# Optimization experiments

Hardware: AMD Instinct MI355X
Metric: run time of the kernel (lower is better)

## Reference

```python
import jax, jax.numpy as jnp
import numpy as np
import math

HIDDEN = 768
NUM_HEADS = 12
HEAD_DIM = HIDDEN // NUM_HEADS
EPS = 1e-05
MU_LEARNED = 0.0    # registered buffer init value (inference mode)
SIGMA_LEARNED = 1.0 # registered buffer init value (inference mode)
SCALES = (0.5, 1.0, 2.0)


def make_pe(n, d):
    # Sinusoidal positional encoding, identical to PositionalEncoding buffer.
    pos = np.arange(n, dtype=np.float32)[:, None]
    div = np.exp(np.arange(0, d, 2, dtype=np.float32) * (-math.log(10000.0) / d))
    pe = np.zeros((n, d), dtype=np.float32)
    pe[:, 0::2] = np.sin(pos * div)
    pe[:, 1::2] = np.cos(pos * div)
    return jnp.asarray(pe)


def setup_inputs() -> dict:
    key = jax.random.key(0)
    ks = jax.random.split(key, 12)
    B, C, Hh, Ww = 8, 256, 32, 32
    feat = jax.random.normal(ks[0], (B, C, Hh, Ww), jnp.float32)
    I = jax.random.uniform(ks[1], (B, 1, Hh, Ww), jnp.float32)
    sc_c = 1.0 / math.sqrt(C)
    sd = 1.0 / math.sqrt(HIDDEN)
    proj_w = jax.random.normal(ks[2], (C, HIDDEN), jnp.float32) * sc_c  # 1x1 conv as matmul
    proj_b = jnp.zeros((HIDDEN,), jnp.float32)
    wq = jax.random.normal(ks[3], (HIDDEN, HIDDEN), jnp.float32) * sd
    bq = jnp.zeros((HIDDEN,), jnp.float32)
    wk = jax.random.normal(ks[4], (HIDDEN, HIDDEN), jnp.float32) * sd
    bk = jnp.zeros((HIDDEN,), jnp.float32)
    wv = jax.random.normal(ks[5], (HIDDEN, HIDDEN), jnp.float32) * sd
    bv = jnp.zeros((HIDDEN,), jnp.float32)
    wo = jax.random.normal(ks[6], (HIDDEN, HIDDEN), jnp.float32) * sd
    bo = jnp.zeros((HIDDEN,), jnp.float32)
    lam = jnp.float32(0.5)
    return dict(feat=feat, I=I, proj_w=proj_w, proj_b=proj_b,
                wq=wq, bq=bq, wk=wk, bk=bk, wv=wv, bv=bv, wo=wo, bo=bo, lam=lam)


def reference(feat, I, proj_w, proj_b, wq, bq, wk, bk, wv, bv, wo, bo, lam):
    B, C, Hh, Ww = feat.shape
    N = Hh * Ww
    # HiddenFeatureProjection: 1x1 conv projection -> flatten -> tokens [B, N, D]
    tokens = jnp.einsum('bchw,cd->bhwd', feat, proj_w).reshape(B, N, HIDDEN) + proj_b
    tokens = tokens + make_pe(N, HIDDEN)[None]
    # GaussianWeightModule (inference path, learned buffers mu=0, sigma=1)
    G = sum(jnp.exp(-(I - MU_LEARNED) ** 2 / (2.0 * (k * SIGMA_LEARNED) ** 2 + EPS))
            for k in SCALES) / float(len(SCALES))  # [B,1,H,W]
    g = G.reshape(B, N)                              # H*W == N by construction
    bias = g[:, :, None] * g[:, None, :]             # [B, N, N] outer product
    # GaussianEnhancedAttention
    q = (tokens @ wq + bq).reshape(B, N, NUM_HEADS, HEAD_DIM).transpose(0, 2, 1, 3)
    k = (tokens @ wk + bk).reshape(B, N, NUM_HEADS, HEAD_DIM).transpose(0, 2, 1, 3)
    v = (tokens @ wv + bv).reshape(B, N, NUM_HEADS, HEAD_DIM).transpose(0, 2, 1, 3)
    scores = jnp.einsum('bhnd,bhmd->bhnm', q, k) / math.sqrt(HEAD_DIM)
    scores = scores + lam * bias[:, None, :, :]
    attn = jax.nn.softmax(scores, axis=-1)
    out = jnp.einsum('bhnm,bhmd->bhnd', attn, v).transpose(0, 2, 1, 3).reshape(B, N, HIDDEN)
    return out @ wo + bo
```

## Files before the change

kernel.cpp:

```cpp
#include <hip/hip_runtime.h>
#include <hip/hip_bf16.h>
#include <math.h>

#define HIDDEN 768
#define NHEADS 12
#define HDIM   64
#define NTOK   1024
#define BATCH  8
#define CIN    256
#define M_ALL  (BATCH * NTOK)
#define LSTR   72

typedef __hip_bfloat16 bf16;
typedef short frag8 __attribute__((ext_vector_type(8)));
typedef short s16x4 __attribute__((ext_vector_type(4)));
typedef unsigned int u32x2 __attribute__((ext_vector_type(2)));
typedef float f32x4 __attribute__((ext_vector_type(4)));

#define GL2LDS(gp, lp) \
    __builtin_amdgcn_global_load_lds((const __attribute__((address_space(1))) void*)(gp), \
                                     (__attribute__((address_space(3))) void*)(lp), 16, 0, 0)

__device__ __forceinline__ short f2bs(float x){
    union { bf16 h; short s; } u; u.h = __float2bfloat16(x); return u.s;
}

__device__ __forceinline__ float gaussw(float x){
    float x2 = x * x;
    return (__expf(-x2 / 0.50001f) + __expf(-x2 / 2.00001f) + __expf(-x2 / 8.00001f)) * (1.0f / 3.0f);
}

__global__ __launch_bounds__(256) void prep_all(
    const float* __restrict__ proj_w, const float* __restrict__ feat,
    short* __restrict__ wtp, short* __restrict__ featT, float* __restrict__ pe)
{
    const int blk = blockIdx.x;
    const int tid = threadIdx.x;
    if (blk >= 560) {
        const float kfac = -9.210340371976184f / 768.0f;
        int e0 = (blk - 560) * 3072 + tid;
        #pragma unroll
        for (int it = 0; it < 12; it++) {
            int e = e0 + it * 256;
            int n = e / 768;
            int d = e - n * 768;
            float ang = (float)n * expf((float)(2 * (d >> 1)) * kfac);
            pe[e] = (d & 1) ? cosf(ang) : sinf(ang);
        }
        return;
    }
    __shared__ short t[64][65];
    const float* W; short* WT; int K, N, k0, n0;
    if (blk < 48) {
        W = proj_w; WT = wtp;
        K = CIN; N = HIDDEN; k0 = (blk / 12) * 64; n0 = (blk % 12) * 64;
    } else {
        int rem = blk - 48;
        int b = rem / 64; rem %= 64;
        W = feat + (size_t)b * CIN * NTOK; WT = featT + (size_t)b * NTOK * CIN;
        K = CIN; N = NTOK; k0 = (rem / 16) * 64; n0 = (rem % 16) * 64;
    }
    #pragma unroll
    for (int it = 0; it < 16; it++) {
        int e = tid + 256 * it;
        int kk = e / 64, nn = e % 64;
        t[kk][nn] = f2bs(W[(size_t)(k0 + kk) * N + n0 + nn]);
    }
    __syncthreads();
    #pragma unroll
    for (int it = 0; it < 16; it++) {
        int e = tid + 256 * it;
        int nn = e / 64, kk = e % 64;
        WT[(size_t)(n0 + nn) * K + k0 + kk] = t[kk][nn];
    }
}

__global__ __launch_bounds__(256) void tokens_wprep(
    const short* __restrict__ A, const short* __restrict__ WT,
    const float* __restrict__ bias, const float* __restrict__ pe,
    short* __restrict__ outv,
    const float* __restrict__ wq, const float* __restrict__ wk,
    const float* __restrict__ wv, const float* __restrict__ wo,
    short* __restrict__ wtqkv)
{
    const int blk = blockIdx.x;
    const int tid = threadIdx.x;
    if (blk >= 768) {
        __shared__ short t[64][65];
        int bw = blk - 768;
        int p = bw / 144, rem = bw % 144;
        const float* srcs[4] = {wq, wk, wv, wo};
        const float* W = srcs[p];
        short* WTo = wtqkv + (size_t)p * HIDDEN * HIDDEN;
        int k0 = (rem / 12) * 64, n0 = (rem % 12) * 64;
        #pragma unroll
        for (int it = 0; it < 16; it++) {
            int e = tid + 256 * it;
            int kk = e / 64, nn = e % 64;
            t[kk][nn] = f2bs(W[(size_t)(k0 + kk) * HIDDEN + n0 + nn]);
        }
        __syncthreads();
        #pragma unroll
        for (int it = 0; it < 16; it++) {
            int e = tid + 256 * it;
            int nn = e / 64, kk = e % 64;
            WTo[(size_t)(n0 + nn) * HIDDEN + k0 + kk] = t[kk][nn];
        }
        return;
    }
    __shared__ short Al[64 * 32];
    __shared__ short Bl[128 * 32];
    const int m0   = (blk & 127) * 64;
    const int n0   = (blk >> 7) * 128;
    const int lane = tid & 63, wid = tid >> 6;
    const int wn   = wid * 32;
    const int l16  = lane & 15, quad = lane >> 4;

    const int sr  = lane >> 2;
    const int ssg = (lane & 3) ^ ((sr >> 1) & 3);
    const int fsw = (l16 >> 1) & 3;

    const f32x4 z4 = {0.f, 0.f, 0.f, 0.f};
    f32x4 acc[4][2];
    #pragma unroll
    for (int i = 0; i < 4; i++)
        #pragma unroll
        for (int j = 0; j < 2; j++) acc[i][j] = z4;

    const int K = CIN;
    for (int k0 = 0; k0 < K; k0 += 32) {
        GL2LDS(A + (size_t)(m0 + wid * 16 + sr) * K + k0 + ssg * 8, &Al[(wid * 16) * 32]);
        #pragma unroll
        for (int t = 0; t < 2; t++) {
            int rbase = wid * 32 + t * 16;
            GL2LDS(WT + (size_t)(n0 + rbase + sr) * K + k0 + ssg * 8, &Bl[rbase * 32]);
        }
        __syncthreads();
        frag8 af[4], bfr[2];
        #pragma unroll
        for (int i = 0; i < 4; i++)
            af[i]  = *(const frag8*)&Al[(i * 16 + l16) * 32 + ((quad ^ fsw) * 8)];
        #pragma unroll
        for (int j = 0; j < 2; j++)
            bfr[j] = *(const frag8*)&Bl[(wn + j * 16 + l16) * 32 + ((quad ^ fsw) * 8)];
        #pragma unroll
        for (int i = 0; i < 4; i++)
            #pragma unroll
            for (int j = 0; j < 2; j++)
                acc[i][j] = __builtin_amdgcn_mfma_f32_16x16x32_bf16(af[i], bfr[j], acc[i][j], 0, 0, 0);
        __syncthreads();
    }

    #pragma unroll
    for (int i = 0; i < 4; i++) {
        #pragma unroll
        for (int r = 0; r < 4; r++) {
            int m = m0 + i * 16 + quad * 4 + r;
            int n_tok = m & (NTOK - 1);
            #pragma unroll
            for (int j = 0; j < 2; j++) {
                int col = n0 + wn + j * 16 + l16;
                float val = acc[i][j][r] + bias[col] + pe[n_tok * HIDDEN + col];
                outv[(size_t)m * HIDDEN + col] = f2bs(val);
            }
        }
    }
}

__global__ __launch_bounds__(256) void transpose_v(
    const short* __restrict__ v, short* __restrict__ vT,
    const float* __restrict__ I, float* __restrict__ g)
{
    if (blockIdx.y == BATCH * NHEADS) {
        int idx = blockIdx.x * 512 + threadIdx.x * 2;
        g[idx]     = gaussw(I[idx]);
        g[idx + 1] = gaussw(I[idx + 1]);
        return;
    }
    __shared__ short t[64][65];
    const int nt = blockIdx.x;
    const int bh = blockIdx.y;
    const int b = bh / NHEADS, h = bh % NHEADS;
    const int tid = threadIdx.x;
    #pragma unroll
    for (int it = 0; it < 16; it++) {
        int e = tid + 256 * it;
        int rr = e / 64, cc = e % 64;
        t[rr][cc] = v[(size_t)(b * NTOK + nt * 64 + rr) * HIDDEN + h * HDIM + cc];
    }
    __syncthreads();
    #pragma unroll
    for (int it = 0; it < 16; it++) {
        int e = tid + 256 * it;
        int c2 = e / 64, r2 = e % 64;
        vT[((size_t)bh * HDIM + c2) * NTOK + nt * 64 + r2] = t[r2][c2];
    }
}

__global__ __launch_bounds__(256) void gemm_mfma128(
    const short* __restrict__ A, const short* __restrict__ WT0, long wt_z,
    const float* __restrict__ b0, const float* __restrict__ b1, const float* __restrict__ b2,
    short* o0, short* o1, short* o2, int K)
{
    __shared__ short Al[2][128 * 32];
    __shared__ short Bl[2][128 * 32];
    const int z = blockIdx.z;
    const short* WT  = WT0 + (size_t)z * wt_z;
    const float* bias = (z == 0) ? b0 : (z == 1) ? b1 : b2;
    short* outv       = (z == 0) ? o0 : (z == 1) ? o1 : o2;

    const int tid  = threadIdx.x;
    const int m0   = blockIdx.x * 128;
    const int n0   = blockIdx.y * 128;
    const int lane = tid & 63, wid = tid >> 6;
    const int wm   = (wid >> 1) * 64, wn = (wid & 1) * 64;
    const int l16  = lane & 15, quad = lane >> 4;

    const int sr  = lane >> 2;
    const int ssg = (lane & 3) ^ ((sr >> 1) & 3);
    const int fsw = (l16 >> 1) & 3;

    const f32x4 z4 = {0.f, 0.f, 0.f, 0.f};
    f32x4 acc[4][4];
    #pragma unroll
    for (int i = 0; i < 4; i++)
        #pragma unroll
        for (int j = 0; j < 4; j++) acc[i][j] = z4;

    #pragma unroll
    for (int t = 0; t < 2; t++) {
        int rbase = wid * 32 + t * 16;
        int r = rbase + sr;
        GL2LDS(A  + (size_t)(m0 + r) * K + ssg * 8, &Al[0][rbase * 32]);
        GL2LDS(WT + (size_t)(n0 + r) * K + ssg * 8, &Bl[0][rbase * 32]);
    }
    __syncthreads();

    const int NSTEP = K / 32;
    for (int ks = 0; ks < NSTEP; ks++) {
        const int cur = ks & 1;
        if (ks < NSTEP - 1) {
            int k0n = (ks + 1) * 32;
            #pragma unroll
            for (int t = 0; t < 2; t++) {
                int rbase = wid * 32 + t * 16;
                int r = rbase + sr;
                GL2LDS(A  + (size_t)(m0 + r) * K + k0n + ssg * 8, &Al[cur ^ 1][rbase * 32]);
                GL2LDS(WT + (size_t)(n0 + r) * K + k0n + ssg * 8, &Bl[cur ^ 1][rbase * 32]);
            }
        }
        frag8 af[4], bfr[4];
        #pragma unroll
        for (int i = 0; i < 4; i++)
            af[i]  = *(const frag8*)&Al[cur][(wm + i * 16 + l16) * 32 + ((quad ^ fsw) * 8)];
        #pragma unroll
        for (int j = 0; j < 4; j++)
            bfr[j] = *(const frag8*)&Bl[cur][(wn + j * 16 + l16) * 32 + ((quad ^ fsw) * 8)];
        #pragma unroll
        for (int i = 0; i < 4; i++)
            #pragma unroll
            for (int j = 0; j < 4; j++)
                acc[i][j] = __builtin_amdgcn_mfma_f32_16x16x32_bf16(af[i], bfr[j], acc[i][j], 0, 0, 0);
        __syncthreads();
    }

    #pragma unroll
    for (int i = 0; i < 4; i++) {
        #pragma unroll
        for (int r = 0; r < 4; r++) {
            int m = m0 + wm + i * 16 + quad * 4 + r;
            #pragma unroll
            for (int j = 0; j < 4; j++) {
                int col = n0 + wn + j * 16 + l16;
                outv[(size_t)m * HIDDEN + col] = f2bs(acc[i][j][r] + bias[col]);
            }
        }
    }
}

__global__ __launch_bounds__(256) void gemm_mfma64f(
    const short* __restrict__ A, const short* __restrict__ WT,
    const float* __restrict__ bias, float* __restrict__ outv, int K)
{
    __shared__ short Al[64 * 32];
    __shared__ short Bl[128 * 32];
    const int tid  = threadIdx.x;
    const int m0   = blockIdx.x * 64;
    const int n0   = blockIdx.y * 128;
    const int lane = tid & 63, wid = tid >> 6;
    const int wn   = wid * 32;
    const int l16  = lane & 15, quad = lane >> 4;

    const int sr  = lane >> 2;
    const int ssg = (lane & 3) ^ ((sr >> 1) & 3);
    const int fsw = (l16 >> 1) & 3;

    const f32x4 z4 = {0.f, 0.f, 0.f, 0.f};
    f32x4 acc[4][2];
    #pragma unroll
    for (int i = 0; i < 4; i++)
        #pragma unroll
        for (int j = 0; j < 2; j++) acc[i][j] = z4;

    for (int k0 = 0; k0 < K; k0 += 32) {
        GL2LDS(A + (size_t)(m0 + wid * 16 + sr) * K + k0 + ssg * 8, &Al[(wid * 16) * 32]);
        #pragma unroll
        for (int t = 0; t < 2; t++) {
            int rbase = wid * 32 + t * 16;
            GL2LDS(WT + (size_t)(n0 + rbase + sr) * K + k0 + ssg * 8, &Bl[rbase * 32]);
        }
        __syncthreads();
        frag8 af[4], bfr[2];
        #pragma unroll
        for (int i = 0; i < 4; i++)
            af[i]  = *(const frag8*)&Al[(i * 16 + l16) * 32 + ((quad ^ fsw) * 8)];
        #pragma unroll
        for (int j = 0; j < 2; j++)
            bfr[j] = *(const frag8*)&Bl[(wn + j * 16 + l16) * 32 + ((quad ^ fsw) * 8)];
        #pragma unroll
        for (int i = 0; i < 4; i++)
            #pragma unroll
            for (int j = 0; j < 2; j++)
                acc[i][j] = __builtin_amdgcn_mfma_f32_16x16x32_bf16(af[i], bfr[j], acc[i][j], 0, 0, 0);
        __syncthreads();
    }

    #pragma unroll
    for (int i = 0; i < 4; i++) {
        #pragma unroll
        for (int r = 0; r < 4; r++) {
            int m = m0 + i * 16 + quad * 4 + r;
            #pragma unroll
            for (int j = 0; j < 2; j++) {
                int col = n0 + wn + j * 16 + l16;
                outv[(size_t)m * HIDDEN + col] = acc[i][j][r] + bias[col];
            }
        }
    }
}

__global__ __launch_bounds__(256, 3) void attn_mfma(
    const short* __restrict__ q, const short* __restrict__ k, const short* __restrict__ vT,
    const float* __restrict__ g, const float* __restrict__ lam_p, short* __restrict__ out)
{
    __shared__ short Pl[128 * LSTR];
    __shared__ short Ks[2][64 * 64];
    __shared__ short Vt[2][64 * 64];

    const int tid  = threadIdx.x;
    const int lin  = blockIdx.x;
    const int xcd  = lin & 7, slot = lin >> 3;
    const int b    = xcd;
    const int h    = slot >> 3;
    const int qt   = slot & 7;
    const float L2E  = 1.4426950408889634f;
    const float lam2 = lam_p[0] * L2E;
    const float scl  = 0.125f * L2E;
    const int lane = tid & 63, wave = tid >> 6;
    const int l16  = lane & 15, quad = lane >> 4;

    const int sr   = lane >> 3;
    const int slin = lane & 7;
    const int ssg  = slin ^ sr;
    const int fsw  = l16 & 7;

    const size_t kb  = (size_t)b * NTOK * HIDDEN + h * HDIM;
    const size_t vtb = (size_t)(b * NHEADS + h) * HDIM * NTOK;
    const float* gk  = g + b * NTOK;

    frag8 aq[2][2];
    #pragma unroll
    for (int half = 0; half < 2; half++)
        #pragma unroll
        for (int kc = 0; kc < 2; kc++)
            aq[half][kc] = *(const frag8*)&q[(size_t)(b * NTOK + qt * 128 + wave * 32 + half * 16 + l16) * HIDDEN
                                             + h * HDIM + kc * 32 + quad * 8];
    float gq[2];
    #pragma unroll
    for (int half = 0; half < 2; half++)
        gq[half] = lam2 * gk[qt * 128 + wave * 32 + half * 16 + l16];

    #pragma unroll
    for (int t = 0; t < 2; t++) {
        int rbase = wave * 16 + t * 8;
        int r = rbase + sr;
        GL2LDS(k  + kb  + (size_t)r * HIDDEN + ssg * 8,  &Ks[0][rbase * 64]);
        GL2LDS(vT + vtb + (size_t)r * NTOK + ssg * 8,    &Vt[0][rbase * 64]);
    }
    __syncthreads();

    const f32x4 z4 = {0.f, 0.f, 0.f, 0.f};
    f32x4 o_acc[2][4];
    #pragma unroll
    for (int half = 0; half < 2; half++)
        #pragma unroll
        for (int d = 0; d < 4; d++) o_acc[half][d] = z4;
    float l_run[2] = {0.f, 0.f};

    for (int jt = 0; jt < 16; jt++) {
        const int cur = jt & 1;
        f32x4 gk4[4];
        #pragma unroll
        for (int t4 = 0; t4 < 4; t4++)
            gk4[t4] = *(const f32x4*)&gk[jt * 64 + t4 * 16 + quad * 4];
        __builtin_amdgcn_sched_barrier(0);
        if (jt < 15) {
            #pragma unroll
            for (int t = 0; t < 2; t++) {
                int rbase = wave * 16 + t * 8;
                int r = rbase + sr;
                GL2LDS(k  + kb  + (size_t)((jt + 1) * 64 + r) * HIDDEN + ssg * 8, &Ks[cur ^ 1][rbase * 64]);
                GL2LDS(vT + vtb + (size_t)r * NTOK + (jt + 1) * 64 + ssg * 8,     &Vt[cur ^ 1][rbase * 64]);
            }
        }

        float p[2][4][4];
        #pragma unroll
        for (int t4 = 0; t4 < 4; t4++) {
            frag8 ak0 = *(const frag8*)&Ks[cur][(t4 * 16 + l16) * 64 + ((quad ^ fsw) * 8)];
            frag8 ak1 = *(const frag8*)&Ks[cur][(t4 * 16 + l16) * 64 + (((quad + 4) ^ fsw) * 8)];
            #pragma unroll
            for (int half = 0; half < 2; half++) {
                f32x4 a = z4;
                a = __builtin_amdgcn_mfma_f32_16x16x32_bf16(ak0, aq[half][0], a, 0, 0, 0);
                a = __builtin_amdgcn_mfma_f32_16x16x32_bf16(ak1, aq[half][1], a, 0, 0, 0);
                #pragma unroll
                for (int r = 0; r < 4; r++) p[half][t4][r] = a[r];
            }
        }

        #pragma unroll
        for (int half = 0; half < 2; half++)
            #pragma unroll
            for (int t4 = 0; t4 < 4; t4++) {
                float e0 = exp2f(fmaf(p[half][t4][0], scl, gq[half] * gk4[t4][0]));
                float e1 = exp2f(fmaf(p[half][t4][1], scl, gq[half] * gk4[t4][1]));
                float e2 = exp2f(fmaf(p[half][t4][2], scl, gq[half] * gk4[t4][2]));
                float e3 = exp2f(fmaf(p[half][t4][3], scl, gq[half] * gk4[t4][3]));
                l_run[half] += (e0 + e1) + (e2 + e3);
                unsigned lo, hi;
                asm("v_cvt_pk_bf16_f32 %0, %1, %2" : "=v"(lo) : "v"(e0), "v"(e1));
                asm("v_cvt_pk_bf16_f32 %0, %1, %2" : "=v"(hi) : "v"(e2), "v"(e3));
                u32x2 w = {lo, hi};
                *(u32x2*)&Pl[(wave * 32 + half * 16 + l16) * LSTR + t4 * 16 + quad * 4] = w;
            }

        frag8 ap[2][2];
        #pragma unroll
        for (int half = 0; half < 2; half++)
            #pragma unroll
            for (int kc = 0; kc < 2; kc++)
                ap[half][kc] = *(const frag8*)&Pl[(wave * 32 + half * 16 + l16) * LSTR + kc * 32 + quad * 8];
        #pragma unroll
        for (int d = 0; d < 4; d++) {
            frag8 av0 = *(const frag8*)&Vt[cur][(d * 16 + l16) * 64 + ((quad ^ fsw) * 8)];
            frag8 av1 = *(const frag8*)&Vt[cur][(d * 16 + l16) * 64 + (((quad + 4) ^ fsw) * 8)];
            #pragma unroll
            for (int half = 0; half < 2; half++) {
                o_acc[half][d] = __builtin_amdgcn_mfma_f32_16x16x32_bf16(ap[half][0], av0, o_acc[half][d], 0, 0, 0);
                o_acc[half][d] = __builtin_amdgcn_mfma_f32_16x16x32_bf16(ap[half][1], av1, o_acc[half][d], 0, 0, 0);
            }
        }
        __syncthreads();
    }

    #pragma unroll
    for (int half = 0; half < 2; half++) {
        float l = l_run[half];
        l += __shfl_xor(l, 16);
        l += __shfl_xor(l, 32);
        #pragma unroll
        for (int r = 0; r < 4; r++) {
            float lq = __shfl(l, (lane & 48) | (quad * 4 + r));
            float inv_l = 1.0f / lq;
            int row = qt * 128 + wave * 32 + half * 16 + quad * 4 + r;
            #pragma unroll
            for (int d = 0; d < 4; d++)
                out[(size_t)(b * NTOK + row) * HIDDEN + h * HDIM + d * 16 + l16]
                    = f2bs(o_acc[half][d][r] * inv_l);
        }
    }
}

extern "C" void kernel_launch(void* const* d_in, const int* in_sizes, int n_in,
                              void* d_out, int out_size, void* d_ws, size_t ws_size,
                              hipStream_t stream)
{
    const float* feat   = (const float*)d_in[0];
    const float* I      = (const float*)d_in[1];
    const float* proj_w = (const float*)d_in[2];
    const float* proj_b = (const float*)d_in[3];
    const float* wq     = (const float*)d_in[4];
    const float* bq     = (const float*)d_in[5];
    const float* wk     = (const float*)d_in[6];
    const float* bk     = (const float*)d_in[7];
    const float* wv     = (const float*)d_in[8];
    const float* bv     = (const float*)d_in[9];
    const float* wo     = (const float*)d_in[10];
    const float* bo     = (const float*)d_in[11];
    const float* lam    = (const float*)d_in[12];
    float* out = (float*)d_out;

    short* wtqkv = (short*)d_ws;
    short* wto   = wtqkv + (size_t)3 * HIDDEN * HIDDEN;
    short* wtp   = wto   + (size_t)HIDDEN * HIDDEN;
    short* tokens= wtp   + (size_t)HIDDEN * CIN;
    short* qbuf  = tokens+ (size_t)M_ALL * HIDDEN;
    short* featT = qbuf;
    float* pebuf = (float*)(qbuf + (size_t)2097152);
    short* vTb   = tokens;
    short* kbuf  = (short*)d_out;
    short* vbuf  = kbuf + (size_t)M_ALL * HIDDEN;
    float* gbuf  = (float*)wtp;

    prep_all<<<816, 256, 0, stream>>>(proj_w, feat, wtp, featT, pebuf);
    tokens_wprep<<<1344, 256, 0, stream>>>(featT, wtp, proj_b, pebuf, tokens,
                                           wq, wk, wv, wo, wtqkv);
    gemm_mfma128<<<dim3(64, 6, 3), 256, 0, stream>>>(tokens, wtqkv, (long)HIDDEN * HIDDEN,
                                                     bq, bk, bv,
                                                     qbuf, kbuf, vbuf, HIDDEN);
    transpose_v<<<dim3(16, 97), 256, 0, stream>>>(vbuf, vTb, I, gbuf);
    attn_mfma<<<768, 256, 0, stream>>>(qbuf, kbuf, vTb, gbuf, lam, qbuf);
    gemm_mfma64f<<<dim3(128, 6), 256, 0, stream>>>(qbuf, wto, bo, out, HIDDEN);
}
```

Baseline: 223.1 us.

## Double-buffer LDS tiles in 64-row GEMMs and vectorize transpose stores

The tokens projection and the output projection GEMMs now keep two LDS buffers per operand and prefetch the next K tile with global_load_lds while the current tile feeds the MFMAs. This hides global-load latency behind compute at the cost of twice the shared memory. Separately, the weight, feature and V transpose kernels switch to 4-wide short vector loads and stores with a padded 68-column tile, cutting the number of memory transactions. The loop body that is not shown must still hold exactly one barrier per iteration for the buffer swap to be safe.

```diff
diff --git a/kernel.cpp b/kernel.cpp
--- a/kernel.cpp
+++ b/kernel.cpp
@@ -49,7 +49,7 @@
         }
         return;
     }
-    __shared__ short t[64][65];
+    __shared__ short t[64][68];
     const float* W; short* WT; int K, N, k0, n0;
     if (blk < 48) {
         W = proj_w; WT = wtp;
@@ -68,10 +68,11 @@
     }
     __syncthreads();
     #pragma unroll
-    for (int it = 0; it < 16; it++) {
-        int e = tid + 256 * it;
-        int nn = e / 64, kk = e % 64;
-        WT[(size_t)(n0 + nn) * K + k0 + kk] = t[kk][nn];
+    for (int it = 0; it < 4; it++) {
+        int idx4 = (tid + 256 * it) * 4;
+        int nn = idx4 / 64, kk = idx4 % 64;
+        s16x4 w = { t[kk][nn], t[kk + 1][nn], t[kk + 2][nn], t[kk + 3][nn] };
+        *(s16x4*)&WT[(size_t)(n0 + nn) * K + k0 + kk] = w;
     }
 }
 
@@ -86,7 +87,7 @@
     const int blk = blockIdx.x;
     const int tid = threadIdx.x;
     if (blk >= 768) {
-        __shared__ short t[64][65];
+        __shared__ short t[64][68];
         int bw = blk - 768;
         int p = bw / 144, rem = bw % 144;
         const float* srcs[4] = {wq, wk, wv, wo};
@@ -101,15 +102,16 @@
         }
         __syncthreads();
         #pragma unroll
-        for (int it = 0; it < 16; it++) {
-            int e = tid + 256 * it;
-            int nn = e / 64, kk = e % 64;
-            WTo[(size_t)(n0 + nn) * HIDDEN + k0 + kk] = t[kk][nn];
+        for (int it = 0; it < 4; it++) {
+            int idx4 = (tid + 256 * it) * 4;
+            int nn = idx4 / 64, kk = idx4 % 64;
+            s16x4 w = { t[kk][nn], t[kk + 1][nn], t[kk + 2][nn], t[kk + 3][nn] };
+            *(s16x4*)&WTo[(size_t)(n0 + nn) * HIDDEN + k0 + kk] = w;
         }
         return;
     }
-    __shared__ short Al[64 * 32];
-    __shared__ short Bl[128 * 32];
+    __shared__ short Al[2][64 * 32];
+    __shared__ short Bl[2][128 * 32];
     const int m0   = (blk & 127) * 64;
     const int n0   = (blk >> 7) * 128;
     const int lane = tid & 63, wid = tid >> 6;
@@ -128,21 +130,33 @@
         for (int j = 0; j < 2; j++) acc[i][j] = z4;
 
     const int K = CIN;
-    for (int k0 = 0; k0 < K; k0 += 32) {
-        GL2LDS(A + (size_t)(m0 + wid * 16 + sr) * K + k0 + ssg * 8, &Al[(wid * 16) * 32]);
-        #pragma unroll
-        for (int t = 0; t < 2; t++) {
-            int rbase = wid * 32 + t * 16;
-            GL2LDS(WT + (size_t)(n0 + rbase + sr) * K + k0 + ssg * 8, &Bl[rbase * 32]);
-        }
-        __syncthreads();
+    GL2LDS(A + (size_t)(m0 + wid * 16 + sr) * K + ssg * 8, &Al[0][(wid * 16) * 32]);
+    #pragma unroll
+    for (int t = 0; t < 2; t++) {
+        int rbase = wid * 32 + t * 16;
+        GL2LDS(WT + (size_t)(n0 + rbase + sr) * K + ssg * 8, &Bl[0][rbase * 32]);
+    }
+    __syncthreads();
+
+    const int NSTEP = K / 32;
+    for (int ks = 0; ks < NSTEP; ks++) {
+        const int cur = ks & 1;
+        if (ks < NSTEP - 1) {
+            int k0n = (ks + 1) * 32;
+            GL2LDS(A + (size_t)(m0 + wid * 16 + sr) * K + k0n + ssg * 8, &Al[cur ^ 1][(wid * 16) * 32]);
+            #pragma unroll
+            for (int t = 0; t < 2; t++) {
+                int rbase = wid * 32 + t * 16;
+                GL2LDS(WT + (size_t)(n0 + rbase + sr) * K + k0n + ssg * 8, &Bl[cur ^ 1][rbase * 32]);
+            }
+        }
         frag8 af[4], bfr[2];
         #pragma unroll
         for (int i = 0; i < 4; i++)
-            af[i]  = *(const frag8*)&Al[(i * 16 + l16) * 32 + ((quad ^ fsw) * 8)];
+            af[i]  = *(const frag8*)&Al[cur][(i * 16 + l16) * 32 + ((quad ^ fsw) * 8)];
         #pragma unroll
         for (int j = 0; j < 2; j++)
-            bfr[j] = *(const frag8*)&Bl[(wn + j * 16 + l16) * 32 + ((quad ^ fsw) * 8)];
+            bfr[j] = *(const frag8*)&Bl[cur][(wn + j * 16 + l16) * 32 + ((quad ^ fsw) * 8)];
         #pragma unroll
         for (int i = 0; i < 4; i++)
             #pragma unroll
@@ -177,23 +191,25 @@
         g[idx + 1] = gaussw(I[idx + 1]);
         return;
     }
-    __shared__ short t[64][65];
+    __shared__ short t[64][68];
     const int nt = blockIdx.x;
     const int bh = blockIdx.y;
     const int b = bh / NHEADS, h = bh % NHEADS;
     const int tid = threadIdx.x;
     #pragma unroll
-    for (int it = 0; it < 16; it++) {
-        int e = tid + 256 * it;
-        int rr = e / 64, cc = e % 64;
-        t[rr][cc] = v[(size_t)(b * NTOK + nt * 64 + rr) * HIDDEN + h * HDIM + cc];
+    for (int it = 0; it < 4; it++) {
+        int idx4 = (tid + 256 * it) * 4;
+        int rr = idx4 / 64, cc = idx4 % 64;
+        *(s16x4*)&t[rr][cc] =
+            *(const s16x4*)&v[(size_t)(b * NTOK + nt * 64 + rr) * HIDDEN + h * HDIM + cc];
     }
     __syncthreads();
     #pragma unroll
-    for (int it = 0; it < 16; it++) {
-        int e = tid + 256 * it;
-        int c2 = e / 64, r2 = e % 64;
-        vT[((size_t)bh * HDIM + c2) * NTOK + nt * 64 + r2] = t[r2][c2];
+    for (int it = 0; it < 4; it++) {
+        int idx4 = (tid + 256 * it) * 4;
+        int c2 = idx4 / 64, r2 = idx4 % 64;
+        s16x4 w = { t[r2][c2], t[r2 + 1][c2], t[r2 + 2][c2], t[r2 + 3][c2] };
+        *(s16x4*)&vT[((size_t)bh * HDIM + c2) * NTOK + nt * 64 + r2] = w;
     }
 }
 
@@ -282,8 +298,8 @@
     const short* __restrict__ A, const short* __restrict__ WT,
     const float* __restrict__ bias, float* __restrict__ outv, int K)
 {
-    __shared__ short Al[64 * 32];
-    __shared__ short Bl[128 * 32];
+    __shared__ short Al[2][64 * 32];
+    __shared__ short Bl[2][128 * 32];
     const int tid  = threadIdx.x;
     const int m0   = blockIdx.x * 64;
     const int n0   = blockIdx.y * 128;
@@ -302,21 +318,33 @@
         #pragma unroll
         for (int j = 0; j < 2; j++) acc[i][j] = z4;
 
-    for (int k0 = 0; k0 < K; k0 += 32) {
-        GL2LDS(A + (size_t)(m0 + wid * 16 + sr) * K + k0 + ssg * 8, &Al[(wid * 16) * 32]);
-        #pragma unroll
-        for (int t = 0; t < 2; t++) {
-            int rbase = wid * 32 + t * 16;
-            GL2LDS(WT + (size_t)(n0 + rbase + sr) * K + k0 + ssg * 8, &Bl[rbase * 32]);
-        }
-        __syncthreads();
+    GL2LDS(A + (size_t)(m0 + wid * 16 + sr) * K + ssg * 8, &Al[0][(wid * 16) * 32]);
+    #pragma unroll
+    for (int t = 0; t < 2; t++) {
+        int rbase = wid * 32 + t * 16;
+        GL2LDS(WT + (size_t)(n0 + rbase + sr) * K + ssg * 8, &Bl[0][rbase * 32]);
+    }
+    __syncthreads();
+
+    const int NSTEP = K / 32;
+    for (int ks = 0; ks < NSTEP; ks++) {
+        const int cur = ks & 1;
+        if (ks < NSTEP - 1) {
+            int k0n = (ks + 1) * 32;
+            GL2LDS(A + (size_t)(m0 + wid * 16 + sr) * K + k0n + ssg * 8, &Al[cur ^ 1][(wid * 16) * 32]);
+            #pragma unroll
+            for (int t = 0; t < 2; t++) {
+                int rbase = wid * 32 + t * 16;
+                GL2LDS(WT + (size_t)(n0 + rbase + sr) * K + k0n + ssg * 8, &Bl[cur ^ 1][rbase * 32]);
+            }
+        }
         frag8 af[4], bfr[2];
         #pragma unroll
         for (int i = 0; i < 4; i++)
-            af[i]  = *(const frag8*)&Al[(i * 16 + l16) * 32 + ((quad ^ fsw) * 8)];
+            af[i]  = *(const frag8*)&Al[cur][(i * 16 + l16) * 32 + ((quad ^ fsw) * 8)];
         #pragma unroll
         for (int j = 0; j < 2; j++)
-            bfr[j] = *(const frag8*)&Bl[(wn + j * 16 + l16) * 32 + ((quad ^ fsw) * 8)];
+            bfr[j] = *(const frag8*)&Bl[cur][(wn + j * 16 + l16) * 32 + ((quad ^ fsw) * 8)];
         #pragma unroll
         for (int i = 0; i < 4; i++)
             #pragma unroll
```

After: 224.6 us. No clear change (+0.6%).
